# Kernel optimization log

Measured on AMD Instinct MI355X. Metric: run time of the kernel, lower is better.

## Reference

```python
import math
import jax, jax.numpy as jnp
import numpy as np
from jax import lax

B, S, D, H, L, F, V = 4, 2048, 768, 12, 6, 3072, 512
HD = D // H
EPS = 1e-5


def setup_inputs():
    key = jax.random.key(0)
    ks = jax.random.split(key, 18)
    std = 0.02
    inp = {
        'x': jax.random.randint(ks[0], (B, S), 0, V, dtype=jnp.int64)
            if jax.config.jax_enable_x64 else jax.random.randint(ks[0], (B, S), 0, V, dtype=jnp.int32),
        'emb': jax.random.normal(ks[1], (V, D), jnp.float32) * std,
        'qkv_w': jax.random.normal(ks[2], (L, D, 3 * D), jnp.float32) * std,
        'qkv_b': jnp.zeros((L, 3 * D), jnp.float32),
        'out_w': jax.random.normal(ks[3], (L, D, D), jnp.float32) * std,
        'out_b': jnp.zeros((L, D), jnp.float32),
        'ln1_s': jnp.ones((L, D), jnp.float32),
        'ln1_b': jnp.zeros((L, D), jnp.float32),
        'w1': jax.random.normal(ks[4], (L, D, F), jnp.float32) * std,
        'b1': jnp.zeros((L, F), jnp.float32),
        'w2': jax.random.normal(ks[5], (L, F, D), jnp.float32) * std,
        'b2': jnp.zeros((L, D), jnp.float32),
        'ln2_s': jnp.ones((L, D), jnp.float32),
        'ln2_b': jnp.zeros((L, D), jnp.float32),
        'lnf_s': jnp.ones((D,), jnp.float32),
        'lnf_b': jnp.zeros((D,), jnp.float32),
        'head_w': jax.random.normal(ks[6], (D, V), jnp.float32) * std,
        'head_b': jnp.zeros((V,), jnp.float32),
    }
    return inp


def _layer_norm(x, s, b):
    mu = jnp.mean(x, -1, keepdims=True)
    var = jnp.mean(jnp.square(x - mu), -1, keepdims=True)
    return (x - mu) * lax.rsqrt(var + EPS) * s + b


def _pos_encoding(seq_len, d_model, dtype):
    pos = jnp.arange(seq_len, dtype=dtype)[:, None]
    div = jnp.exp(jnp.arange(0, d_model, 2, dtype=dtype) * (-math.log(10000.0) / d_model))
    pe = jnp.zeros((seq_len, d_model), dtype)
    pe = pe.at[:, 0::2].set(jnp.sin(pos * div))
    pe = pe.at[:, 1::2].set(jnp.cos(pos * div))
    return pe


def reference(x, emb, qkv_w, qkv_b, out_w, out_b, ln1_s, ln1_b,
              w1, b1, w2, b2, ln2_s, ln2_b, lnf_s, lnf_b, head_w, head_b):
    b, s = x.shape
    d = emb.shape[1]
    h = emb[x] * math.sqrt(d)                      # [B,S,D]
    h = h + _pos_encoding(s, d, h.dtype)
    causal = jnp.tril(jnp.ones((s, s), bool))      # [S,S]
    scale = HD ** -0.5

    def block(hcarry, p):
        qw, qb, ow, ob, l1s, l1b, w1i, b1i, w2i, b2i, l2s, l2b = p
        xn = _layer_norm(hcarry, l1s, l1b)
        qkv = xn @ qw + qb                          # [B,S,3D]
        qkv = qkv.reshape(b, s, 3, H, HD).transpose(2, 0, 3, 1, 4)
        q, k, v = qkv[0], qkv[1], qkv[2]            # each [B,H,S,hd]
        scores = jnp.einsum('bhqd,bhkd->bhqk', q, k) * scale
        scores = jnp.where(causal, scores, -jnp.inf)
        attn = jax.nn.softmax(scores, axis=-1)
        o = jnp.einsum('bhqk,bhkd->bhqd', attn, v)
        o = o.transpose(0, 2, 1, 3).reshape(b, s, d)
        hcarry = hcarry + (o @ ow + ob)
        xn2 = _layer_norm(hcarry, l2s, l2b)
        ff = jax.nn.relu(xn2 @ w1i + b1i) @ w2i + b2i
        return hcarry + ff, None

    h, _ = lax.scan(block, h, (qkv_w, qkv_b, out_w, out_b, ln1_s, ln1_b,
                               w1, b1, w2, b2, ln2_s, ln2_b))
    h = _layer_norm(h, lnf_s, lnf_b)
    return h @ head_w + head_b                     # [B,S,V]
```

## Files before the change

### kernel.cpp

```cpp
#include <hip/hip_runtime.h>
#include <math.h>
#include <stdio.h>

#define Bv 4
#define Sv 2048
#define Dv 768
#define Hv 12
#define Lv 6
#define Fv 3072
#define Vv 512
#define Mv (Bv*Sv)

typedef __bf16 bf16;
typedef __bf16 bf16x8 __attribute__((ext_vector_type(8)));
typedef __bf16 bf16x4 __attribute__((ext_vector_type(4)));
typedef short  s16x4  __attribute__((ext_vector_type(4)));
typedef float  f32x4  __attribute__((ext_vector_type(4)));

__device__ __forceinline__ void gload_lds16(const void* g, void* l) {
  __builtin_amdgcn_global_load_lds(
      (__attribute__((address_space(1))) void*)(void*)g,
      (__attribute__((address_space(3))) void*)l, 16, 0, 0);
}

__device__ __forceinline__ int xcd_remap(int orig, int nwg) {
  int q = nwg >> 3, r = nwg & 7;
  int xcd = orig & 7, loc = orig >> 3;
  return (xcd < r ? xcd * (q + 1) : r * (q + 1) + (xcd - r) * q) + loc;
}

__global__ void detect_i64(const int* __restrict__ x, int* __restrict__ flag) {
  __shared__ int red[256];
  int acc = 0;
  for (int i = threadIdx.x; i < Mv / 2; i += 256) acc |= x[2 * i + 1];
  red[threadIdx.x] = acc;
  __syncthreads();
  for (int s = 128; s > 0; s >>= 1) {
    if (threadIdx.x < s) red[threadIdx.x] |= red[threadIdx.x + s];
    __syncthreads();
  }
  if (threadIdx.x == 0) *flag = (red[0] == 0) ? 1 : 0;
}

__global__ void embed_kernel(const int* __restrict__ x, const float* __restrict__ emb,
                             float* __restrict__ h, const int* __restrict__ i64flag) {
  int idx = blockIdx.x * 256 + threadIdx.x;
  int j  = idx % (Dv / 2);
  int bs = idx / (Dv / 2);
  int s  = bs % Sv;
  int tok = (*i64flag) ? x[2 * bs] : x[bs];
  float2 e = *(const float2*)(emb + (size_t)tok * Dv + 2 * j);
  float div = expf((float)(2 * j) * (-9.210340371976184f / (float)Dv));
  float arg = (float)s * div;
  const float sq = 27.712812921102035f;
  float2 o;
  o.x = e.x * sq + sinf(arg);
  o.y = e.y * sq + cosf(arg);
  *(float2*)(h + (size_t)bs * Dv + 2 * j) = o;
}

__global__ void transpose_cvt(const float* __restrict__ in, bf16* __restrict__ out,
                              int K, int N) {
  __shared__ float tile[64][65];
  in  += (size_t)blockIdx.z * K * N;
  out += (size_t)blockIdx.z * K * N;
  int n0 = blockIdx.x * 64, k0 = blockIdx.y * 64;
  int tx = threadIdx.x & 63, ty = threadIdx.x >> 6;
#pragma unroll
  for (int i = 0; i < 64; i += 4)
    tile[ty + i][tx] = in[(size_t)(k0 + ty + i) * N + n0 + tx];
  __syncthreads();
#pragma unroll
  for (int i = 0; i < 64; i += 4)
    out[(size_t)(n0 + ty + i) * K + k0 + tx] = (bf16)tile[tx][ty + i];
}

__global__ void vtrans(const bf16* __restrict__ qkv, bf16* __restrict__ vt) {
  __shared__ bf16 tile[64][72];
  const int st = blockIdx.x;
  const int bh = blockIdx.y;
  const int b = bh / Hv, h = bh % Hv;
  const bf16* src = qkv + ((size_t)b * Sv + st * 64) * 2304 + 1536 + h * 64;
  const int rl = threadIdx.x >> 3;
  const int c8 = (threadIdx.x & 7) * 8;
#pragma unroll
  for (int i = 0; i < 2; ++i) {
    bf16x8 v = *(const bf16x8*)(src + (size_t)(rl + i * 32) * 2304 + c8);
    *(bf16x8*)&tile[rl + i * 32][c8] = v;
  }
  __syncthreads();
  bf16* dst = vt + ((size_t)bh * 64) * Sv + st * 64;
#pragma unroll
  for (int i = 0; i < 2; ++i) {
    bf16 tmp[8];
#pragma unroll
    for (int j = 0; j < 8; ++j) tmp[j] = tile[c8 + j][rl + i * 32];
    *(bf16x8*)(dst + (size_t)(rl + i * 32) * Sv + c8) = *(bf16x8*)tmp;
  }
}

__global__ void ln_kernel(const float* __restrict__ hin, const float* __restrict__ sc,
                          const float* __restrict__ bi, bf16* __restrict__ out) {
  int row  = blockIdx.x * 4 + (threadIdx.x >> 6);
  int lane = threadIdx.x & 63;
  const float* p = hin + (size_t)row * Dv + lane * 12;
  float v[12];
  *(float4*)(v)     = *(const float4*)(p);
  *(float4*)(v + 4) = *(const float4*)(p + 4);
  *(float4*)(v + 8) = *(const float4*)(p + 8);
  float sum = 0.f, sq = 0.f;
#pragma unroll
  for (int j = 0; j < 12; ++j) { sum += v[j]; sq += v[j] * v[j]; }
#pragma unroll
  for (int m = 1; m < 64; m <<= 1) {
    sum += __shfl_xor(sum, m, 64);
    sq  += __shfl_xor(sq,  m, 64);
  }
  float mu  = sum * (1.f / 768.f);
  float var = sq * (1.f / 768.f) - mu * mu;
  float rs  = rsqrtf(var + 1e-5f);
  float s_[12], b_[12];
  const float* scp = sc + lane * 12;
  const float* bip = bi + lane * 12;
  *(float4*)(s_)     = *(const float4*)(scp);
  *(float4*)(s_ + 4) = *(const float4*)(scp + 4);
  *(float4*)(s_ + 8) = *(const float4*)(scp + 8);
  *(float4*)(b_)     = *(const float4*)(bip);
  *(float4*)(b_ + 4) = *(const float4*)(bip + 4);
  *(float4*)(b_ + 8) = *(const float4*)(bip + 8);
  union { bf16 h2[12]; uint2 q[3]; } ob;
#pragma unroll
  for (int j = 0; j < 12; ++j)
    ob.h2[j] = (bf16)((v[j] - mu) * rs * s_[j] + b_[j]);
  uint2* op = (uint2*)(out + (size_t)row * Dv + lane * 12);
  op[0] = ob.q[0]; op[1] = ob.q[1]; op[2] = ob.q[2];
}

template<bool RELU, bool RESID, int OUTMODE>
__global__ __launch_bounds__(256) void gemm_bt(
    const bf16* __restrict__ A, const bf16* __restrict__ Bt,
    const float* __restrict__ bias, float* __restrict__ hres,
    bf16* __restrict__ outb, float* __restrict__ outf, int M, int N, int K) {
  __shared__ bf16 sA[2][128 * 64];
  __shared__ bf16 sB[2][128 * 64];
  const int gx = gridDim.x;
  const int wg = xcd_remap(blockIdx.y * gx + blockIdx.x, gx * gridDim.y);
  const int bn = (wg % gx) * 128, bm = (wg / gx) * 128;
  const int t = threadIdx.x, lane = t & 63, wid = t >> 6;
  const int wr = wid >> 1, wc = wid & 1;
  const int g = lane >> 4, c = lane & 15;
  f32x4 acc[4][4];
#pragma unroll
  for (int i = 0; i < 4; ++i)
#pragma unroll
    for (int j = 0; j < 4; ++j) acc[i][j] = (f32x4){0.f, 0.f, 0.f, 0.f};
  const int nkt = K >> 6;

  auto stage = [&](int bb, int kt) {
#pragma unroll
    for (int j2 = 0; j2 < 4; ++j2) {
      int ch  = t + j2 * 256;
      int row = ch >> 3;
      int src = ((ch & 7) * 8) ^ ((row & 7) << 3);
      gload_lds16(A  + (size_t)(bm + row) * K + kt * 64 + src, &sA[bb][ch * 8]);
      gload_lds16(Bt + (size_t)(bn + row) * K + kt * 64 + src, &sB[bb][ch * 8]);
    }
  };

  stage(0, 0);
  const int swz = (c & 7) << 3;
  for (int kt = 0; kt < nkt; ++kt) {
    const int cb = kt & 1;
    if (kt + 1 < nkt) {
      stage(cb ^ 1, kt + 1);
      asm volatile("s_waitcnt vmcnt(8)" ::: "memory");
    } else {
      asm volatile("s_waitcnt vmcnt(0)" ::: "memory");
    }
    __builtin_amdgcn_s_barrier();
    __builtin_amdgcn_sched_barrier(0);
#pragma unroll
    for (int f = 0; f < 2; ++f) {
      bf16x8 aF[4], bF[4];
      const int e = (f * 32 + g * 8) ^ swz;
#pragma unroll
      for (int mt = 0; mt < 4; ++mt)
        aF[mt] = *(const bf16x8*)&sA[cb][(wr * 64 + mt * 16 + c) * 64 + e];
#pragma unroll
      for (int nt = 0; nt < 4; ++nt)
        bF[nt] = *(const bf16x8*)&sB[cb][(wc * 64 + nt * 16 + c) * 64 + e];
      __builtin_amdgcn_s_setprio(1);
#pragma unroll
      for (int mt = 0; mt < 4; ++mt)
#pragma unroll
        for (int nt = 0; nt < 4; ++nt)
          acc[mt][nt] = __builtin_amdgcn_mfma_f32_16x16x32_bf16(
              aF[mt], bF[nt], acc[mt][nt], 0, 0, 0);
      __builtin_amdgcn_s_setprio(0);
    }
    __builtin_amdgcn_sched_barrier(0);
    __builtin_amdgcn_s_barrier();
  }
#pragma unroll
  for (int nt = 0; nt < 4; ++nt) {
    int col = bn + wc * 64 + nt * 16 + c;
    float bv = bias[col];
#pragma unroll
    for (int mt = 0; mt < 4; ++mt) {
      int row0 = bm + wr * 64 + mt * 16 + g * 4;
#pragma unroll
      for (int r = 0; r < 4; ++r) {
        float vv = acc[mt][nt][r] + bv;
        if (RELU) vv = fmaxf(vv, 0.f);
        size_t off = (size_t)(row0 + r) * N + col;
        if (RESID) { vv += hres[off]; hres[off] = vv; }
        if (OUTMODE == 1) outb[off] = (bf16)vv;
        if (OUTMODE == 2) outf[off] = vv;
      }
    }
  }
}

template<bool RELU, bool RESID, int OUTMODE>
__global__ __launch_bounds__(256) void gemm_sk(
    const bf16* __restrict__ A, const bf16* __restrict__ Bt,
    const float* __restrict__ bias, float* __restrict__ hres,
    bf16* __restrict__ outb, float* __restrict__ outf, int M, int N, int K) {
  __shared__ bf16 sA[2][64 * 64];
  __shared__ bf16 sB[2][128 * 64];
  const int gx = gridDim.x;
  const int wg = xcd_remap(blockIdx.y * gx + blockIdx.x, gx * gridDim.y);
  const int bn = (wg % gx) * 128, bm = (wg / gx) * 64;
  const int t = threadIdx.x, lane = t & 63, wid = t >> 6;
  const int wr = wid >> 1, wc = wid & 1;
  const int g = lane >> 4, c = lane & 15;
  f32x4 acc[2][4];
#pragma unroll
  for (int i = 0; i < 2; ++i)
#pragma unroll
    for (int j = 0; j < 4; ++j) acc[i][j] = (f32x4){0.f, 0.f, 0.f, 0.f};
  const int nkt = K >> 6;

  auto stage = [&](int bb, int kt) {
#pragma unroll
    for (int j2 = 0; j2 < 2; ++j2) {
      int ch  = t + j2 * 256;
      int row = ch >> 3;
      int src = ((ch & 7) * 8) ^ ((row & 7) << 3);
      gload_lds16(A + (size_t)(bm + row) * K + kt * 64 + src, &sA[bb][ch * 8]);
    }
#pragma unroll
    for (int j2 = 0; j2 < 4; ++j2) {
      int ch  = t + j2 * 256;
      int row = ch >> 3;
      int src = ((ch & 7) * 8) ^ ((row & 7) << 3);
      gload_lds16(Bt + (size_t)(bn + row) * K + kt * 64 + src, &sB[bb][ch * 8]);
    }
  };

  stage(0, 0);
  const int swz = (c & 7) << 3;
  for (int kt = 0; kt < nkt; ++kt) {
    const int cb = kt & 1;
    if (kt + 1 < nkt) {
      stage(cb ^ 1, kt + 1);
      asm volatile("s_waitcnt vmcnt(6)" ::: "memory");
    } else {
      asm volatile("s_waitcnt vmcnt(0)" ::: "memory");
    }
    __builtin_amdgcn_s_barrier();
    __builtin_amdgcn_sched_barrier(0);
#pragma unroll
    for (int f = 0; f < 2; ++f) {
      bf16x8 aF[2], bF[4];
      const int e = (f * 32 + g * 8) ^ swz;
#pragma unroll
      for (int mt = 0; mt < 2; ++mt)
        aF[mt] = *(const bf16x8*)&sA[cb][(wr * 32 + mt * 16 + c) * 64 + e];
#pragma unroll
      for (int nt = 0; nt < 4; ++nt)
        bF[nt] = *(const bf16x8*)&sB[cb][(wc * 64 + nt * 16 + c) * 64 + e];
      __builtin_amdgcn_s_setprio(1);
#pragma unroll
      for (int mt = 0; mt < 2; ++mt)
#pragma unroll
        for (int nt = 0; nt < 4; ++nt)
          acc[mt][nt] = __builtin_amdgcn_mfma_f32_16x16x32_bf16(
              aF[mt], bF[nt], acc[mt][nt], 0, 0, 0);
      __builtin_amdgcn_s_setprio(0);
    }
    __builtin_amdgcn_sched_barrier(0);
    __builtin_amdgcn_s_barrier();
  }
#pragma unroll
  for (int nt = 0; nt < 4; ++nt) {
    int col = bn + wc * 64 + nt * 16 + c;
    float bv = bias[col];
#pragma unroll
    for (int mt = 0; mt < 2; ++mt) {
      int row0 = bm + wr * 32 + mt * 16 + g * 4;
#pragma unroll
      for (int r = 0; r < 4; ++r) {
        float vv = acc[mt][nt][r] + bv;
        if (RELU) vv = fmaxf(vv, 0.f);
        size_t off = (size_t)(row0 + r) * N + col;
        if (RESID) { vv += hres[off]; hres[off] = vv; }
        if (OUTMODE == 1) outb[off] = (bf16)vv;
        if (OUTMODE == 2) outf[off] = vv;
      }
    }
  }
}

__global__ __launch_bounds__(256) void attn_kernel(const bf16* __restrict__ qkv,
                                                   const bf16* __restrict__ vt,
                                                   bf16* __restrict__ o) {
  __shared__ bf16 sK[2][64 * 64], sVT[2][64 * 64];
  const int nwg = 16 * Bv * Hv;
  const int wgl = xcd_remap(blockIdx.y * 16 + blockIdx.x, nwg);
  const int i  = wgl % 16;
  const int bh = wgl / 16;
  const int qtA = i, qtB = 31 - i;
  const int b  = bh / Hv;
  const int h  = bh % Hv;
  const int t = threadIdx.x, lane = t & 63, wid = t >> 6;
  const int g = lane >> 4, c = lane & 15;
  const int QST = 2304;
  const bf16* qbase  = qkv + (size_t)b * Sv * QST + h * 64;
  const bf16* vtbase = vt + ((size_t)bh * 64) * Sv;
  const float CS = 0.18033688011112042f;
  const float THR = 11.541560327111707f;
  const int swz = (c & 7) << 3;

  bf16x8 qfA[2], qfB[2];
  {
    const bf16* qa = qbase + (size_t)(qtA * 64 + wid * 16 + c) * QST;
    qfA[0] = *(const bf16x8*)(qa + g * 8);
    qfA[1] = *(const bf16x8*)(qa + 32 + g * 8);
    const bf16* qb = qbase + (size_t)(qtB * 64 + wid * 16 + c) * QST;
    qfB[0] = *(const bf16x8*)(qb + g * 8);
    qfB[1] = *(const bf16x8*)(qb + 32 + g * 8);
  }
  f32x4 accA[4], accB[4];
  float mA = -INFINITY, lA = 0.f, mB = -INFINITY, lB = 0.f;
#pragma unroll
  for (int d0 = 0; d0 < 4; ++d0) {
    accA[d0] = (f32x4){0.f, 0.f, 0.f, 0.f};
    accB[d0] = (f32x4){0.f, 0.f, 0.f, 0.f};
  }
  const int qlA = qtA * 64 + wid * 16 + c;
  const int qlB = qtB * 64 + wid * 16 + c;

  auto stage = [&](int bb, int kt) {
#pragma unroll
    for (int j2 = 0; j2 < 2; ++j2) {
      int ch  = t + j2 * 256;
      int row = ch >> 3;
      int src = ((ch & 7) * 8) ^ ((row & 7) << 3);
      gload_lds16(qbase + (size_t)(kt * 64 + row) * QST + 768 + src, &sK[bb][ch * 8]);
      gload_lds16(vtbase + (size_t)row * Sv + kt * 64 + src, &sVT[bb][ch * 8]);
    }
  };

  auto process = [&](int bb, const bf16x8* qf, f32x4* accO, float& m_s, float& l_s,
                     int ql, int kt, bool diag) {
    f32x4 accT[4];
#pragma unroll
    for (int nt = 0; nt < 4; ++nt) accT[nt] = (f32x4){0.f, 0.f, 0.f, 0.f};
    __builtin_amdgcn_s_setprio(1);
#pragma unroll
    for (int nt = 0; nt < 4; ++nt)
#pragma unroll
      for (int f = 0; f < 2; ++f) {
        bf16x8 kf = *(const bf16x8*)&sK[bb][(nt * 16 + c) * 64 + ((f * 32 + g * 8) ^ swz)];
        accT[nt] = __builtin_amdgcn_mfma_f32_16x16x32_bf16(kf, qf[f], accT[nt], 0, 0, 0);
      }
    __builtin_amdgcn_s_setprio(0);
#pragma unroll
    for (int nt = 0; nt < 4; ++nt)
#pragma unroll
      for (int r = 0; r < 4; ++r) accT[nt][r] *= CS;
    if (diag) {
#pragma unroll
      for (int nt = 0; nt < 4; ++nt)
#pragma unroll
        for (int r = 0; r < 4; ++r)
          if ((kt * 64 + nt * 16 + g * 4 + r) > ql) accT[nt][r] = -INFINITY;
    }
    float mt = -INFINITY;
#pragma unroll
    for (int nt = 0; nt < 4; ++nt)
#pragma unroll
      for (int r = 0; r < 4; ++r) mt = fmaxf(mt, accT[nt][r]);
    mt = fmaxf(mt, __shfl_xor(mt, 16, 64));
    mt = fmaxf(mt, __shfl_xor(mt, 32, 64));
    const bool skip = __all(mt <= m_s + THR);
    const float mn = skip ? m_s : fmaxf(m_s, mt);
    float ps = 0.f;
#pragma unroll
    for (int nt = 0; nt < 4; ++nt)
#pragma unroll
      for (int r = 0; r < 4; ++r) {
        float p = __builtin_amdgcn_exp2f(accT[nt][r] - mn);
        accT[nt][r] = p;
        ps += p;
      }
    ps += __shfl_xor(ps, 16, 64);
    ps += __shfl_xor(ps, 32, 64);
    if (skip) {
      l_s += ps;
    } else {
      float al = __builtin_amdgcn_exp2f(m_s - mn);
      m_s = mn;
      l_s = l_s * al + ps;
#pragma unroll
      for (int r = 0; r < 4; ++r) {
        float alq = __shfl(al, g * 4 + r, 64);
#pragma unroll
        for (int d0 = 0; d0 < 4; ++d0) accO[d0][r] *= alq;
      }
    }
    s16x4 pa[4];
#pragma unroll
    for (int nt = 0; nt < 4; ++nt) {
      bf16x4 pb;
#pragma unroll
      for (int r = 0; r < 4; ++r) pb[r] = (bf16)accT[nt][r];
      pa[nt] = __builtin_bit_cast(s16x4, pb);
    }
    __builtin_amdgcn_s_setprio(1);
#pragma unroll
    for (int d0 = 0; d0 < 4; ++d0) {
      const int drow = (d0 * 16 + c) * 64;
#pragma unroll
      for (int nt = 0; nt < 4; ++nt) {
        int chunk = (nt * 2 + (g >> 1)) ^ (c & 7);
        s16x4 vfr = *(const s16x4*)&sVT[bb][drow + chunk * 8 + (g & 1) * 4];
        accO[d0] = __builtin_amdgcn_mfma_f32_16x16x16bf16_1k(pa[nt], vfr, accO[d0], 0, 0, 0);
      }
    }
    __builtin_amdgcn_s_setprio(0);
  };

  stage(0, 0);
  int cur = 0;
  for (int kt = 0; kt <= qtB; ++kt) {
    __syncthreads();
    if (kt < qtB) stage(cur ^ 1, kt + 1);
    if (kt <= qtA) process(cur, qfA, accA, mA, lA, qlA, kt, kt == qtA);
    process(cur, qfB, accB, mB, lB, qlB, kt, kt == qtB);
    cur ^= 1;
  }

  float invA = 1.f / lA, invB = 1.f / lB;
#pragma unroll
  for (int r = 0; r < 4; ++r) {
    float iA = __shfl(invA, g * 4 + r, 64);
    float iB = __shfl(invB, g * 4 + r, 64);
    size_t orA = (size_t)b * Sv + qtA * 64 + wid * 16 + g * 4 + r;
    size_t orB = (size_t)b * Sv + qtB * 64 + wid * 16 + g * 4 + r;
#pragma unroll
    for (int d0 = 0; d0 < 4; ++d0) {
      o[orA * Dv + h * 64 + d0 * 16 + c] = (bf16)(accA[d0][r] * iA);
      o[orB * Dv + h * 64 + d0 * 16 + c] = (bf16)(accB[d0][r] * iB);
    }
  }
}

extern "C" void kernel_launch(void* const* d_in, const int* in_sizes, int n_in,
                              void* d_out, int out_size, void* d_ws, size_t ws_size,
                              hipStream_t stream) {
  const int*   x     = (const int*)d_in[0];
  const float* emb   = (const float*)d_in[1];
  const float* qkv_w = (const float*)d_in[2];
  const float* qkv_b = (const float*)d_in[3];
  const float* out_w = (const float*)d_in[4];
  const float* out_b = (const float*)d_in[5];
  const float* ln1_s = (const float*)d_in[6];
  const float* ln1_b = (const float*)d_in[7];
  const float* w1    = (const float*)d_in[8];
  const float* b1    = (const float*)d_in[9];
  const float* w2    = (const float*)d_in[10];
  const float* b2    = (const float*)d_in[11];
  const float* ln2_s = (const float*)d_in[12];
  const float* ln2_b = (const float*)d_in[13];
  const float* lnf_s = (const float*)d_in[14];
  const float* lnf_b = (const float*)d_in[15];
  const float* head_w= (const float*)d_in[16];
  const float* head_b= (const float*)d_in[17];
  float* out = (float*)d_out;
  (void)in_sizes; (void)n_in; (void)out_size;

  char* ws = (char*)d_ws;
  size_t off = 0;
  auto alloc = [&](size_t bytes) -> char* {
    char* p = ws + off; off += (bytes + 255) & ~(size_t)255; return p;
  };
  float* hbuf  = (float*)alloc((size_t)Mv * Dv * 4);
  bf16*  xn    = (bf16*) alloc((size_t)Mv * Dv * 2);
  bf16*  qkvff = (bf16*) alloc((size_t)Mv * Fv * 2);
  bf16*  vt    = (bf16*) alloc((size_t)Bv * Hv * 64 * Sv * 2);
  bf16*  attn_o= (bf16*) alloc((size_t)Mv * Dv * 2);
  bf16*  qkvT  = (bf16*) alloc((size_t)Lv * 3 * Dv * Dv * 2);
  bf16*  outT  = (bf16*) alloc((size_t)Lv * Dv * Dv * 2);
  bf16*  w1T   = (bf16*) alloc((size_t)Lv * Fv * Dv * 2);
  bf16*  w2T   = (bf16*) alloc((size_t)Lv * Fv * Dv * 2);
  bf16*  headT = (bf16*) alloc((size_t)Vv * Dv * 2);
  int*   i64f  = (int*)  alloc(256);

  fprintf(stderr, "[kernel_launch] ws_size=%zu needed=%zu out_size=%d\n",
          ws_size, off, out_size);
  if (off > ws_size) {
    fprintf(stderr, "[kernel_launch] WORKSPACE TOO SMALL - not launching\n");
    return;
  }

  detect_i64<<<1, 256, 0, stream>>>(x, i64f);
  transpose_cvt<<<dim3(36, 12, Lv), 256, 0, stream>>>(qkv_w, qkvT, Dv, 3 * Dv);
  transpose_cvt<<<dim3(12, 12, Lv), 256, 0, stream>>>(out_w, outT, Dv, Dv);
  transpose_cvt<<<dim3(48, 12, Lv), 256, 0, stream>>>(w1, w1T, Dv, Fv);
  transpose_cvt<<<dim3(12, 48, Lv), 256, 0, stream>>>(w2, w2T, Fv, Dv);
  transpose_cvt<<<dim3(8, 12, 1), 256, 0, stream>>>(head_w, headT, Dv, Vv);
  embed_kernel<<<Mv * (Dv / 2) / 256, 256, 0, stream>>>(x, emb, hbuf, i64f);

  for (int l = 0; l < Lv; ++l) {
    ln_kernel<<<Mv / 4, 256, 0, stream>>>(hbuf, ln1_s + l * Dv, ln1_b + l * Dv, xn);
    gemm_bt<false, false, 1><<<dim3(3 * Dv / 128, Mv / 128), 256, 0, stream>>>(
        xn, qkvT + (size_t)l * 3 * Dv * Dv, qkv_b + l * 3 * Dv, nullptr, qkvff,
        nullptr, Mv, 3 * Dv, Dv);
    vtrans<<<dim3(Sv / 64, Bv * Hv), 256, 0, stream>>>(qkvff, vt);
    attn_kernel<<<dim3(16, Bv * Hv), 256, 0, stream>>>(qkvff, vt, attn_o);
    gemm_sk<false, true, 0><<<dim3(Dv / 128, Mv / 64), 256, 0, stream>>>(
        attn_o, outT + (size_t)l * Dv * Dv, out_b + l * Dv, hbuf, nullptr,
        nullptr, Mv, Dv, Dv);
    ln_kernel<<<Mv / 4, 256, 0, stream>>>(hbuf, ln2_s + l * Dv, ln2_b + l * Dv, xn);
    gemm_bt<true, false, 1><<<dim3(Fv / 128, Mv / 128), 256, 0, stream>>>(
        xn, w1T + (size_t)l * Fv * Dv, b1 + l * Fv, nullptr, qkvff, nullptr,
        Mv, Fv, Dv);
    gemm_sk<false, true, 0><<<dim3(Dv / 128, Mv / 64), 256, 0, stream>>>(
        qkvff, w2T + (size_t)l * Fv * Dv, b2 + l * Dv, hbuf, nullptr, nullptr,
        Mv, Dv, Fv);
  }
  ln_kernel<<<Mv / 4, 256, 0, stream>>>(hbuf, lnf_s, lnf_b, xn);
  gemm_sk<false, false, 2><<<dim3(Vv / 128, Mv / 64), 256, 0, stream>>>(
      xn, headT, head_b, nullptr, nullptr, out, Mv, Vv, Dv);
}
```

Before: 1.637 ms.

## Split paired-query-tile attention blocks into one query tile per workgroup

The attention kernel used to pair query tiles i and 31-i in a single workgroup so every block did the same amount of causal work. It now launches 32 workgroups per (batch, head), each handling one query tile, with the heaviest tiles scheduled first. This doubles the grid (768 blocks) for better occupancy and fewer live registers per block, but K/V tiles shared by the pair are now loaded twice and the per-block work becomes uneven. The scale multiply is also folded into the exp2 argument through an fma, and the running max is scaled once.

```diff
diff --git a/kernel.cpp b/kernel.cpp
--- a/kernel.cpp
+++ b/kernel.cpp
@@ -316,11 +316,10 @@
                                                    const bf16* __restrict__ vt,
                                                    bf16* __restrict__ o) {
   __shared__ bf16 sK[2][64 * 64], sVT[2][64 * 64];
-  const int nwg = 16 * Bv * Hv;
-  const int wgl = xcd_remap(blockIdx.y * 16 + blockIdx.x, nwg);
-  const int i  = wgl % 16;
-  const int bh = wgl / 16;
-  const int qtA = i, qtB = 31 - i;
+  const int nwg = 32 * Bv * Hv;
+  const int wgl = xcd_remap(blockIdx.y * 32 + blockIdx.x, nwg);
+  const int qt = 31 - (wgl & 31);
+  const int bh = wgl >> 5;
   const int b  = bh / Hv;
   const int h  = bh % Hv;
   const int t = threadIdx.x, lane = t & 63, wid = t >> 6;
@@ -332,24 +331,17 @@
   const float THR = 11.541560327111707f;
   const int swz = (c & 7) << 3;
 
-  bf16x8 qfA[2], qfB[2];
+  bf16x8 qf[2];
   {
-    const bf16* qa = qbase + (size_t)(qtA * 64 + wid * 16 + c) * QST;
-    qfA[0] = *(const bf16x8*)(qa + g * 8);
-    qfA[1] = *(const bf16x8*)(qa + 32 + g * 8);
-    const bf16* qb = qbase + (size_t)(qtB * 64 + wid * 16 + c) * QST;
-    qfB[0] = *(const bf16x8*)(qb + g * 8);
-    qfB[1] = *(const bf16x8*)(qb + 32 + g * 8);
-  }
-  f32x4 accA[4], accB[4];
-  float mA = -INFINITY, lA = 0.f, mB = -INFINITY, lB = 0.f;
-#pragma unroll
-  for (int d0 = 0; d0 < 4; ++d0) {
-    accA[d0] = (f32x4){0.f, 0.f, 0.f, 0.f};
-    accB[d0] = (f32x4){0.f, 0.f, 0.f, 0.f};
-  }
-  const int qlA = qtA * 64 + wid * 16 + c;
-  const int qlB = qtB * 64 + wid * 16 + c;
+    const bf16* qa = qbase + (size_t)(qt * 64 + wid * 16 + c) * QST;
+    qf[0] = *(const bf16x8*)(qa + g * 8);
+    qf[1] = *(const bf16x8*)(qa + 32 + g * 8);
+  }
+  f32x4 accO[4];
+  float m_s = -INFINITY, l_s = 0.f;
+#pragma unroll
+  for (int d0 = 0; d0 < 4; ++d0) accO[d0] = (f32x4){0.f, 0.f, 0.f, 0.f};
+  const int ql = qt * 64 + wid * 16 + c;
 
   auto stage = [&](int bb, int kt) {
 #pragma unroll
@@ -362,8 +354,7 @@
     }
   };
 
-  auto process = [&](int bb, const bf16x8* qf, f32x4* accO, float& m_s, float& l_s,
-                     int ql, int kt, bool diag) {
+  auto process = [&](int bb, int kt, bool diag) {
     f32x4 accT[4];
 #pragma unroll
     for (int nt = 0; nt < 4; ++nt) accT[nt] = (f32x4){0.f, 0.f, 0.f, 0.f};
@@ -376,10 +367,6 @@
         accT[nt] = __builtin_amdgcn_mfma_f32_16x16x32_bf16(kf, qf[f], accT[nt], 0, 0, 0);
       }
     __builtin_amdgcn_s_setprio(0);
-#pragma unroll
-    for (int nt = 0; nt < 4; ++nt)
-#pragma unroll
-      for (int r = 0; r < 4; ++r) accT[nt][r] *= CS;
     if (diag) {
 #pragma unroll
       for (int nt = 0; nt < 4; ++nt)
@@ -392,6 +379,7 @@
     for (int nt = 0; nt < 4; ++nt)
 #pragma unroll
       for (int r = 0; r < 4; ++r) mt = fmaxf(mt, accT[nt][r]);
+    mt *= CS;
     mt = fmaxf(mt, __shfl_xor(mt, 16, 64));
     mt = fmaxf(mt, __shfl_xor(mt, 32, 64));
     const bool skip = __all(mt <= m_s + THR);
@@ -401,7 +389,7 @@
     for (int nt = 0; nt < 4; ++nt)
 #pragma unroll
       for (int r = 0; r < 4; ++r) {
-        float p = __builtin_amdgcn_exp2f(accT[nt][r] - mn);
+        float p = __builtin_amdgcn_exp2f(fmaf(accT[nt][r], CS, -mn));
         accT[nt][r] = p;
         ps += p;
       }
@@ -444,26 +432,21 @@
 
   stage(0, 0);
   int cur = 0;
-  for (int kt = 0; kt <= qtB; ++kt) {
+  for (int kt = 0; kt <= qt; ++kt) {
     __syncthreads();
-    if (kt < qtB) stage(cur ^ 1, kt + 1);
-    if (kt <= qtA) process(cur, qfA, accA, mA, lA, qlA, kt, kt == qtA);
-    process(cur, qfB, accB, mB, lB, qlB, kt, kt == qtB);
+    if (kt < qt) stage(cur ^ 1, kt + 1);
+    process(cur, kt, kt == qt);
     cur ^= 1;
   }
 
-  float invA = 1.f / lA, invB = 1.f / lB;
+  float inv = 1.f / l_s;
 #pragma unroll
   for (int r = 0; r < 4; ++r) {
-    float iA = __shfl(invA, g * 4 + r, 64);
-    float iB = __shfl(invB, g * 4 + r, 64);
-    size_t orA = (size_t)b * Sv + qtA * 64 + wid * 16 + g * 4 + r;
-    size_t orB = (size_t)b * Sv + qtB * 64 + wid * 16 + g * 4 + r;
-#pragma unroll
-    for (int d0 = 0; d0 < 4; ++d0) {
-      o[orA * Dv + h * 64 + d0 * 16 + c] = (bf16)(accA[d0][r] * iA);
-      o[orB * Dv + h * 64 + d0 * 16 + c] = (bf16)(accB[d0][r] * iB);
-    }
+    float iq = __shfl(inv, g * 4 + r, 64);
+    size_t orow = (size_t)b * Sv + qt * 64 + wid * 16 + g * 4 + r;
+#pragma unroll
+    for (int d0 = 0; d0 < 4; ++d0)
+      o[orow * Dv + h * 64 + d0 * 16 + c] = (bf16)(accO[d0][r] * iq);
   }
 }
 
@@ -529,7 +512,7 @@
         xn, qkvT + (size_t)l * 3 * Dv * Dv, qkv_b + l * 3 * Dv, nullptr, qkvff,
         nullptr, Mv, 3 * Dv, Dv);
     vtrans<<<dim3(Sv / 64, Bv * Hv), 256, 0, stream>>>(qkvff, vt);
-    attn_kernel<<<dim3(16, Bv * Hv), 256, 0, stream>>>(qkvff, vt, attn_o);
+    attn_kernel<<<dim3(32, Bv * Hv), 256, 0, stream>>>(qkvff, vt, attn_o);
     gemm_sk<false, true, 0><<<dim3(Dv / 128, Mv / 64), 256, 0, stream>>>(
         attn_o, outT + (size_t)l * Dv * Dv, out_b + l * Dv, hbuf, nullptr,
         nullptr, Mv, Dv, Dv);
```

Result: slower. 1.688 ms (+3.1%).
